# Performance work log

Hardware: AMD Instinct MI355X
Metric: run time of the kernel (lower is better)

Reference implementation:

```python
import jax, jax.numpy as jnp
import numpy as np

B, S, H, T, W = 8, 512, 768, 4, 10
NEG = -1e9

def _u(key, shape, k):
    return jax.random.uniform(key, shape, jnp.float32, -k, k)

def setup_inputs():
    key = jax.random.key(0)
    ks = jax.random.split(key, 20)
    kh = float(1.0 / np.sqrt(H)); kt = float(1.0 / np.sqrt(T))
    return dict(
        embeddings=jax.random.normal(ks[0], (B, S, H), jnp.float32),
        l1f_wih=_u(ks[1], (4 * H, H), kh), l1f_whh=_u(ks[2], (4 * H, H), kh), l1f_b=_u(ks[3], (4 * H,), kh),
        l1r_wih=_u(ks[4], (4 * H, H), kh), l1r_whh=_u(ks[5], (4 * H, H), kh), l1r_b=_u(ks[6], (4 * H,), kh),
        attn_w=_u(ks[7], (3 * H,), kh), attn_b=_u(ks[8], (1,), kh),
        l2f_wih=_u(ks[9], (4 * T, 2 * H), kt), l2f_whh=_u(ks[10], (4 * T, T), kt), l2f_b=_u(ks[11], (4 * T,), kt),
        l2r_wih=_u(ks[12], (4 * T, 2 * H), kt), l2r_whh=_u(ks[13], (4 * T, T), kt), l2r_b=_u(ks[14], (4 * T,), kt),
        crf_start=0.1 * jax.random.normal(ks[15], (T,), jnp.float32),
        crf_end=0.1 * jax.random.normal(ks[16], (T,), jnp.float32),
        crf_trans=0.1 * jax.random.normal(ks[17], (T, T), jnp.float32),
        window_size=W,
    )

def _lstm_dir(x, w_ih, w_hh, b):
    # x: [B,S,D] -> [B,S,Hh]; torch gate order i,f,g,o
    Hh = w_hh.shape[1]
    bs = x.shape[0]
    xs = (jnp.einsum('bsd,gd->bsg', x, w_ih) + b).transpose(1, 0, 2)  # [S,B,4Hh]
    def step(carry, xt):
        h, c = carry
        g = xt + h @ w_hh.T
        i, f, gg, o = jnp.split(g, 4, axis=-1)
        c = jax.nn.sigmoid(f) * c + jax.nn.sigmoid(i) * jnp.tanh(gg)
        h = jax.nn.sigmoid(o) * jnp.tanh(c)
        return (h, c), h
    init = (jnp.zeros((bs, Hh), x.dtype), jnp.zeros((bs, Hh), x.dtype))
    _, hs = jax.lax.scan(step, init, xs)
    return hs.transpose(1, 0, 2)

def _bilstm(x, pf, pr):
    hf = _lstm_dir(x, *pf)
    hr = _lstm_dir(x[:, ::-1], *pr)[:, ::-1]
    return jnp.concatenate([hf, hr], axis=-1)

def _win_attn(h, w, b, win):
    # h: [B,S,D]; similarity(hi,hj) = w1.hi + w2.hj + w3.(hi*hj) + b
    bs, s, d = h.shape
    w1, w2, w3 = w[:d], w[d:2 * d], w[2 * d:]
    offs = jnp.arange(-win, win + 1)                      # [K]
    idx = jnp.arange(s)[:, None] + offs[None, :]          # [S,K]
    valid = (idx >= 0) & (idx < s)
    idxc = jnp.clip(idx, 0, s - 1)
    hw = h[:, idxc]                                       # [B,S,K,D]
    scores = (h @ w1)[:, :, None] \
        + jnp.einsum('bskd,d->bsk', hw, w2) \
        + jnp.einsum('bsd,bskd->bsk', h * w3, hw) + b[0]
    scores = jnp.where(valid[None], scores, NEG)
    aw = jax.nn.softmax(scores, axis=-1)                  # [B,S,K]
    return jnp.einsum('bsk,bskd->bsd', aw, hw)

def _viterbi(em, start, end, trans):
    # em: [B,S,T] -> tags [B,S]
    score0 = start[None] + em[:, 0]
    ems = em.transpose(1, 0, 2)[1:]                       # [S-1,B,T]
    def step(score, e_t):
        nxt = score[:, :, None] + trans[None]             # [B,Tprev,T]
        best = jnp.max(nxt, axis=1) + e_t
        bp = jnp.argmax(nxt, axis=1)
        return best, bp
    final, bps = jax.lax.scan(step, score0, ems)          # bps [S-1,B,T]
    final = final + end[None]
    last = jnp.argmax(final, axis=-1)                     # [B]
    def back(tag, bp):
        prev = jnp.take_along_axis(bp, tag[:, None], axis=1)[:, 0]
        return prev, prev
    _, tags_rev = jax.lax.scan(back, last, bps[::-1])
    return jnp.concatenate([tags_rev[::-1], last[None]], axis=0).transpose(1, 0)

def reference(embeddings, l1f_wih, l1f_whh, l1f_b, l1r_wih, l1r_whh, l1r_b,
              attn_w, attn_b, l2f_wih, l2f_whh, l2f_b, l2r_wih, l2r_whh, l2r_b,
              crf_start, crf_end, crf_trans, window_size):
    h1 = _bilstm(embeddings, (l1f_wih, l1f_whh, l1f_b), (l1r_wih, l1r_whh, l1r_b))
    d = h1.shape[-1] // 2
    hs = h1[..., :d] + h1[..., d:]                        # sum of directions [B,S,H]
    att = _win_attn(hs, attn_w, attn_b, int(window_size))
    x2 = jnp.concatenate([hs, att], axis=-1)              # [B,S,2H]
    h2 = _bilstm(x2, (l2f_wih, l2f_whh, l2f_b), (l2r_wih, l2r_whh, l2r_b))
    d2 = h2.shape[-1] // 2
    em = h2[..., :d2] + h2[..., d2:]                      # CRF emissions [B,S,T]
    tags = _viterbi(em, crf_start, crf_end, crf_trans)
    return tags, em
```

## Files before the change

kernel.cpp:

```cpp
#include <hip/hip_runtime.h>
#include <math.h>

#define SEQ 512
#define BATCH 8
#define HID 768
#define G4 3072
#define CHUNK 128
#define NEGV (-1000000000.0f)

typedef float v4f __attribute__((ext_vector_type(4)));

__device__ __forceinline__ float sigm(float x) { return 1.0f / (1.0f + expf(-x)); }

__device__ __forceinline__ float wred(float x) {
#pragma unroll
  for (int off = 32; off > 0; off >>= 1) x += __shfl_xor(x, off, 64);
  return x;
}

__device__ __forceinline__ void load2_f4_sc(const float* p0, const float* p1,
                                            v4f& a, v4f& b) {
  asm volatile("global_load_dwordx4 %0, %2, off sc0 sc1\n\t"
               "global_load_dwordx4 %1, %3, off sc0 sc1\n\t"
               "s_waitcnt vmcnt(0)"
               : "=&v"(a), "=&v"(b) : "v"(p0), "v"(p1) : "memory");
}
__device__ __forceinline__ int load_i_sc(const int* p) {
  int r;
  asm volatile("global_load_dword %0, %1, off sc0 sc1\n\ts_waitcnt vmcnt(0)"
               : "=v"(r) : "v"(p) : "memory");
  return r;
}
__device__ __forceinline__ void store_f_sc(float* p, float v) {
  asm volatile("global_store_dword %0, %1, off sc0 sc1" :: "v"(p), "v"(v) : "memory");
}
__device__ __forceinline__ void store_i_sc(int* p, int v) {
  asm volatile("global_store_dword %0, %1, off sc0 sc1" :: "v"(p), "v"(v) : "memory");
}

template <int CTRL, int RMASK>
__device__ __forceinline__ float dpp_add(float x) {
  int y = __builtin_amdgcn_update_dpp(0, __float_as_int(x), CTRL, RMASK, 0xF, false);
  return x + __int_as_float(y);
}
__device__ __forceinline__ float reduce32(float x) {
  x = dpp_add<0x121, 0xF>(x);
  x = dpp_add<0x122, 0xF>(x);
  x = dpp_add<0x124, 0xF>(x);
  x = dpp_add<0x128, 0xF>(x);
  x = dpp_add<0x142, 0xA>(x);
  return x;
}

__global__ void k_init(float* __restrict__ hbuf, int* __restrict__ flags) {
  int i = blockIdx.x * blockDim.x + threadIdx.x;
  if (i < 2 * 2 * BATCH * HID) hbuf[i] = 0.0f;
  if (i < 4096) flags[i] = 0;
}

__global__ __launch_bounds__(256) void k_proj1(
    const float* __restrict__ emb,
    const float* __restrict__ w_f, const float* __restrict__ b_f,
    const float* __restrict__ w_r, const float* __restrict__ b_r,
    float* __restrict__ xs_f, float* __restrict__ xs_r, int chunk) {
  __shared__ float As[16][132];
  __shared__ float Bs[16][132];
  const int tid = threadIdx.x;
  const int bn0 = blockIdx.x * 128;
  const int bb  = blockIdx.y;
  const int dir = blockIdx.z;
  const float* W    = dir ? w_r : w_f;
  const float* bias = dir ? b_r : b_f;
  float* xs = dir ? xs_r : xs_f;

  float acc[8][8];
#pragma unroll
  for (int i = 0; i < 8; i++)
#pragma unroll
    for (int j = 0; j < 8; j++) acc[i][j] = 0.0f;

  const int mload = tid & 127;
  const int kq0   = tid >> 7;
  const int tglob = dir ? (SEQ - 1 - (chunk * CHUNK + mload)) : (chunk * CHUNK + mload);
  const float* arow = emb + (size_t)(bb * SEQ + tglob) * HID;
  const float* brow = W + (size_t)(bn0 + mload) * HID;
  const int tm = tid & 15, tn = tid >> 4;

  for (int kt = 0; kt < HID; kt += 16) {
#pragma unroll
    for (int rep = 0; rep < 2; rep++) {
      int kq = kq0 + rep * 2;
      float4 a = *(const float4*)(arow + kt + kq * 4);
      As[kq * 4 + 0][mload] = a.x; As[kq * 4 + 1][mload] = a.y;
      As[kq * 4 + 2][mload] = a.z; As[kq * 4 + 3][mload] = a.w;
      float4 b = *(const float4*)(brow + kt + kq * 4);
      Bs[kq * 4 + 0][mload] = b.x; Bs[kq * 4 + 1][mload] = b.y;
      Bs[kq * 4 + 2][mload] = b.z; Bs[kq * 4 + 3][mload] = b.w;
    }
    __syncthreads();
#pragma unroll
    for (int k = 0; k < 16; k++) {
      float4 a0 = *(const float4*)&As[k][tm * 8];
      float4 a1 = *(const float4*)&As[k][tm * 8 + 4];
      float4 b0 = *(const float4*)&Bs[k][tn * 8];
      float4 b1 = *(const float4*)&Bs[k][tn * 8 + 4];
      float av[8] = {a0.x, a0.y, a0.z, a0.w, a1.x, a1.y, a1.z, a1.w};
      float bv[8] = {b0.x, b0.y, b0.z, b0.w, b1.x, b1.y, b1.z, b1.w};
#pragma unroll
      for (int i = 0; i < 8; i++)
#pragma unroll
        for (int j = 0; j < 8; j++) acc[i][j] += av[i] * bv[j];
    }
    __syncthreads();
  }
#pragma unroll
  for (int i = 0; i < 8; i++) {
    int row = tm * 8 + i;
    size_t base = (size_t)(bb * CHUNK + row) * G4 + bn0 + tn * 8;
#pragma unroll
    for (int j = 0; j < 8; j++) xs[base + j] = acc[i][j] + bias[bn0 + tn * 8 + j];
  }
}

__global__ __launch_bounds__(384, 2) void k_rec1(
    const float* __restrict__ whh_f, const float* __restrict__ whh_r,
    const float* __restrict__ xs_f, const float* __restrict__ xs_r,
    float* __restrict__ hbuf, float* __restrict__ cbuf, int* __restrict__ flags,
    float* __restrict__ hf, float* __restrict__ hr, int t0, int init) {
  __shared__ float hlds[4 * HID];
  const int tid = threadIdx.x;
  const int bid = blockIdx.x;
  const int dir = bid >> 7;
  const int bh  = (bid >> 6) & 1;
  const int jb  = bid & 63;
  const int J0  = jb * 12;
  const int grp = dir * 2 + bh;
  const int g  = tid >> 5;
  const int kq = tid & 31;
  const int j  = J0 + g;

  const float* W  = dir ? whh_r : whh_f;
  const float* xs = dir ? xs_r  : xs_f;
  float* harr = dir ? hr : hf;

  float wreg[4][24];
#pragma unroll
  for (int gate = 0; gate < 4; gate++) {
#pragma unroll
    for (int q = 0; q < 6; q++) {
      *(v4f*)&wreg[gate][q * 4] =
          *(const v4f*)&W[(size_t)(gate * HID + j) * HID + q * 128 + kq * 4];
    }
  }

  float cc[4];
#pragma unroll
  for (int b = 0; b < 4; b++) cc[b] = 0.0f;
  if (!init && kq == 16) {
#pragma unroll
    for (int b = 0; b < 4; b++) cc[b] = cbuf[bid * 48 + g * 4 + b];
  }

  for (int stp = 0; stp < CHUNK; stp++) {
    const int s = t0 + stp;
    const int par = s & 1;

    float xsv[4][4];
    if (kq == 16) {
#pragma unroll
      for (int b = 0; b < 4; b++) {
        const size_t xbase = (size_t)((bh * 4 + b) * CHUNK + stp) * G4 + j;
#pragma unroll
        for (int gate = 0; gate < 4; gate++)
          xsv[b][gate] = xs[xbase + gate * HID];
      }
    }

    if (tid < 64) {
      const int* fp = flags + (grp * 64 + tid) * 16;
      while (load_i_sc(fp) < s) { __builtin_amdgcn_s_sleep(4); }
    }
    __syncthreads();

    {
      const float* src = hbuf + (size_t)((par * 2 + dir) * BATCH + bh * 4) * HID + tid * 8;
      v4f a, b4;
      load2_f4_sc(src, src + 4, a, b4);
      *(v4f*)&hlds[tid * 8]     = a;
      *(v4f*)&hlds[tid * 8 + 4] = b4;
    }
    __syncthreads();

    float acc[4][4];
#pragma unroll
    for (int gate = 0; gate < 4; gate++)
#pragma unroll
      for (int b = 0; b < 4; b++) acc[gate][b] = 0.0f;
#pragma unroll
    for (int b = 0; b < 4; b++) {
      float hk[24];
#pragma unroll
      for (int q = 0; q < 6; q++)
        *(v4f*)&hk[q * 4] = *(const v4f*)&hlds[b * HID + q * 128 + kq * 4];
#pragma unroll
      for (int gate = 0; gate < 4; gate++)
#pragma unroll
        for (int k = 0; k < 24; k++) acc[gate][b] += wreg[gate][k] * hk[k];
    }
#pragma unroll
    for (int gate = 0; gate < 4; gate++)
#pragma unroll
      for (int b = 0; b < 4; b++) acc[gate][b] = reduce32(acc[gate][b]);

    if (kq == 16) {
      const int t = dir ? (SEQ - 1 - s) : s;
#pragma unroll
      for (int b = 0; b < 4; b++) {
        const int bg = bh * 4 + b;
        float iv = acc[0][b] + xsv[b][0];
        float fv = acc[1][b] + xsv[b][1];
        float gv = acc[2][b] + xsv[b][2];
        float ov = acc[3][b] + xsv[b][3];
        cc[b] = sigm(fv) * cc[b] + sigm(iv) * tanhf(gv);
        float h = sigm(ov) * tanhf(cc[b]);
        store_f_sc(hbuf + (size_t)(((par ^ 1) * 2 + dir) * BATCH + bg) * HID + j, h);
        harr[(size_t)(bg * SEQ + t) * HID + j] = h;
      }
    }
    asm volatile("s_waitcnt vmcnt(0)" ::: "memory");
    __syncthreads();
    if (tid == 0) store_i_sc(flags + (grp * 64 + jb) * 16, s + 1);
  }
  if (kq == 16) {
#pragma unroll
    for (int b = 0; b < 4; b++) cbuf[bid * 48 + g * 4 + b] = cc[b];
  }
}

__global__ void k_sum(float* __restrict__ hf, const float* __restrict__ hr) {
  int i = blockIdx.x * 256 + threadIdx.x;
  float4 a = ((const float4*)hf)[i];
  float4 b = ((const float4*)hr)[i];
  a.x += b.x; a.y += b.y; a.z += b.z; a.w += b.w;
  ((float4*)hf)[i] = a;
}

__global__ __launch_bounds__(64) void k_attn(
    const float* __restrict__ hs, const float* __restrict__ attn_w,
    const float* __restrict__ attn_b, float* __restrict__ att) {
  const int l = threadIdx.x;
  const int s = blockIdx.x, b = blockIdx.y;
  const float* hrow = hs + (size_t)(b * SEQ + s) * HID;
  float v[12];
  float u1p = 0.0f;
#pragma unroll
  for (int jj = 0; jj < 12; jj++) {
    int d = l + 64 * jj;
    float x = hrow[d];
    u1p += x * attn_w[d];
    v[jj] = attn_w[HID + d] + x * attn_w[2 * HID + d];
  }
  float u1 = wred(u1p) + attn_b[0];
  float sc[21];
  for (int o = 0; o < 21; o++) {
    int s2 = s + o - 10;
    if (s2 >= 0 && s2 < SEQ) {
      const float* h2 = hs + (size_t)(b * SEQ + s2) * HID;
      float p = 0.0f;
#pragma unroll
      for (int jj = 0; jj < 12; jj++) p += h2[l + 64 * jj] * v[jj];
      sc[o] = wred(p) + u1;
    } else {
      sc[o] = NEGV;
    }
  }
  float m = sc[0];
#pragma unroll
  for (int o = 1; o < 21; o++) m = fmaxf(m, sc[o]);
  float sum = 0.0f;
#pragma unroll
  for (int o = 0; o < 21; o++) { sc[o] = expf(sc[o] - m); sum += sc[o]; }
  float inv = 1.0f / sum;
  float acc[12];
#pragma unroll
  for (int jj = 0; jj < 12; jj++) acc[jj] = 0.0f;
  for (int o = 0; o < 21; o++) {
    int s2 = s + o - 10;
    if (s2 < 0 || s2 >= SEQ) continue;
    float a = sc[o] * inv;
    const float* h2 = hs + (size_t)(b * SEQ + s2) * HID;
#pragma unroll
    for (int jj = 0; jj < 12; jj++) acc[jj] += a * h2[l + 64 * jj];
  }
  float* orow = att + (size_t)(b * SEQ + s) * HID;
#pragma unroll
  for (int jj = 0; jj < 12; jj++) orow[l + 64 * jj] = acc[jj];
}

__global__ __launch_bounds__(256) void k_proj2(
    const float* __restrict__ hs, const float* __restrict__ att,
    const float* __restrict__ w2f, const float* __restrict__ b2f,
    const float* __restrict__ w2r, const float* __restrict__ b2r,
    float* __restrict__ xs2) {
  __shared__ __align__(16) float x2[2 * HID];
  __shared__ float part[32][9];
  const int tid = threadIdx.x;
  const int s = blockIdx.x, b = blockIdx.y;
  size_t base = (size_t)(b * SEQ + s) * HID;
  for (int i = tid; i < 2 * HID; i += 256)
    x2[i] = (i < HID) ? hs[base + i] : att[base + i - HID];
  __syncthreads();
  const int gid = tid & 31, pp = tid >> 5;
  const int d = gid >> 4, g = gid & 15;
  const float4* w4 = (const float4*)((d ? w2r : w2f) + (size_t)g * (2 * HID));
  const float4* x4 = (const float4*)x2;
  float p = 0.0f;
  for (int e = pp * 48; e < pp * 48 + 48; e++) {
    float4 xv = x4[e];
    float4 wv = w4[e];
    p += xv.x * wv.x + xv.y * wv.y + xv.z * wv.z + xv.w * wv.w;
  }
  part[gid][pp] = p;
  __syncthreads();
  if (tid < 32) {
    float sumv = (d ? b2r : b2f)[g];
#pragma unroll
    for (int q = 0; q < 8; q++) sumv += part[gid][q];
    xs2[(size_t)((d * BATCH + b) * SEQ + s) * 16 + g] = sumv;
  }
}

__global__ __launch_bounds__(256) void k_rec2(
    const float* __restrict__ xs2,
    const float* __restrict__ whh_f, const float* __restrict__ whh_r,
    float* __restrict__ h2) {
  __shared__ float hsh[2 * BATCH * 4];
  __shared__ float gsh[2 * BATCH * 16];
  const int tid = threadIdx.x;
  const int d = tid >> 7, b = (tid >> 4) & 7, g = tid & 15;
  const float* whh = (d ? whh_r : whh_f) + g * 4;
  const float w0 = whh[0], w1 = whh[1], w2 = whh[2], w3 = whh[3];
  const int hb = d * BATCH + b;
  if (g < 4) hsh[hb * 4 + g] = 0.0f;
  float c = 0.0f;
  __syncthreads();
  const float* xrow = xs2 + (size_t)hb * SEQ * 16 + g;
  for (int st = 0; st < SEQ; st++) {
    int t = d ? (SEQ - 1 - st) : st;
    float gv = xrow[t * 16] + w0 * hsh[hb * 4 + 0] + w1 * hsh[hb * 4 + 1] +
               w2 * hsh[hb * 4 + 2] + w3 * hsh[hb * 4 + 3];
    gsh[hb * 16 + g] = gv;
    __syncthreads();
    if (g < 4) {
      float iv = gsh[hb * 16 + g];
      float fv = gsh[hb * 16 + 4 + g];
      float gq = gsh[hb * 16 + 8 + g];
      float ov = gsh[hb * 16 + 12 + g];
      c = sigm(fv) * c + sigm(iv) * tanhf(gq);
      float h = sigm(ov) * tanhf(c);
      hsh[hb * 4 + g] = h;
      h2[((size_t)hb * SEQ + t) * 4 + g] = h;
    }
    __syncthreads();
  }
}

__global__ void k_em(const float* __restrict__ h2, float* __restrict__ out) {
  int i = blockIdx.x * 256 + threadIdx.x;
  if (i < BATCH * SEQ * 4) out[BATCH * SEQ + i] = h2[i] + h2[BATCH * SEQ * 4 + i];
}

__global__ __launch_bounds__(32) void k_viterbi(
    float* __restrict__ out, const float* __restrict__ start,
    const float* __restrict__ endw, const float* __restrict__ trans) {
  __shared__ unsigned char bp[SEQ - 1][32];
  const int l = threadIdx.x;
  const int b = l >> 2, j = l & 3;
  const float* em = out + BATCH * SEQ;
  const float tr0 = trans[0 * 4 + j], tr1 = trans[1 * 4 + j];
  const float tr2 = trans[2 * 4 + j], tr3 = trans[3 * 4 + j];
  float score = start[j] + em[((size_t)b * SEQ + 0) * 4 + j];
  for (int t = 1; t < SEQ; t++) {
    float s0 = __shfl(score, b * 4 + 0, 64);
    float s1 = __shfl(score, b * 4 + 1, 64);
    float s2 = __shfl(score, b * 4 + 2, 64);
    float s3 = __shfl(score, b * 4 + 3, 64);
    float v0 = s0 + tr0, v1 = s1 + tr1, v2 = s2 + tr2, v3 = s3 + tr3;
    float best = v0; int arg = 0;
    if (v1 > best) { best = v1; arg = 1; }
    if (v2 > best) { best = v2; arg = 2; }
    if (v3 > best) { best = v3; arg = 3; }
    bp[t - 1][l] = (unsigned char)arg;
    score = best + em[((size_t)b * SEQ + t) * 4 + j];
  }
  score += endw[j];
  float f0 = __shfl(score, b * 4 + 0, 64);
  float f1 = __shfl(score, b * 4 + 1, 64);
  float f2 = __shfl(score, b * 4 + 2, 64);
  float f3 = __shfl(score, b * 4 + 3, 64);
  if (j == 0) {
    float bbv = f0; int last = 0;
    if (f1 > bbv) { bbv = f1; last = 1; }
    if (f2 > bbv) { bbv = f2; last = 2; }
    if (f3 > bbv) { bbv = f3; last = 3; }
    int tag = last;
    out[b * SEQ + (SEQ - 1)] = (float)tag;
    for (int t = SEQ - 2; t >= 0; t--) {
      tag = bp[t][b * 4 + tag];
      out[b * SEQ + t] = (float)tag;
    }
  }
}

extern "C" void kernel_launch(void* const* d_in, const int* in_sizes, int n_in,
                              void* d_out, int out_size, void* d_ws, size_t ws_size,
                              hipStream_t stream) {
  const float* emb      = (const float*)d_in[0];
  const float* l1f_wih  = (const float*)d_in[1];
  const float* l1f_whh  = (const float*)d_in[2];
  const float* l1f_b    = (const float*)d_in[3];
  const float* l1r_wih  = (const float*)d_in[4];
  const float* l1r_whh  = (const float*)d_in[5];
  const float* l1r_b    = (const float*)d_in[6];
  const float* attn_w   = (const float*)d_in[7];
  const float* attn_b   = (const float*)d_in[8];
  const float* l2f_wih  = (const float*)d_in[9];
  const float* l2f_whh  = (const float*)d_in[10];
  const float* l2f_b    = (const float*)d_in[11];
  const float* l2r_wih  = (const float*)d_in[12];
  const float* l2r_whh  = (const float*)d_in[13];
  const float* l2r_b    = (const float*)d_in[14];
  const float* crf_start= (const float*)d_in[15];
  const float* crf_end  = (const float*)d_in[16];
  const float* crf_trans= (const float*)d_in[17];

  float* ws = (float*)d_ws;
  const size_t NCH = (size_t)BATCH * CHUNK * G4;
  float* xs_f = ws;
  float* xs_r = xs_f + NCH;
  float* hf   = xs_r + NCH;
  float* hr   = hf + (size_t)BATCH * SEQ * HID;
  float* hbuf = hr + (size_t)BATCH * SEQ * HID;
  float* cbuf = hbuf + 2 * 2 * BATCH * HID;
  float* h2   = cbuf + 256 * 48;
  int*   flags= (int*)(h2 + 2 * BATCH * SEQ * 4);
  float* xs2  = xs_f;
  float* att  = xs_r;
  float* hs   = hf;

  k_init<<<dim3(96), dim3(256), 0, stream>>>(hbuf, flags);

  for (int c = 0; c < 4; c++) {
    k_proj1<<<dim3(24, 8, 2), dim3(256), 0, stream>>>(
        emb, l1f_wih, l1f_b, l1r_wih, l1r_b, xs_f, xs_r, c);
    k_rec1<<<dim3(256), dim3(384), 0, stream>>>(
        l1f_whh, l1r_whh, xs_f, xs_r, hbuf, cbuf, flags, hf, hr,
        c * CHUNK, c == 0 ? 1 : 0);
  }

  k_sum<<<dim3(3072), dim3(256), 0, stream>>>(hf, hr);
  k_attn<<<dim3(SEQ, BATCH), dim3(64), 0, stream>>>(hs, attn_w, attn_b, att);
  k_proj2<<<dim3(SEQ, BATCH), dim3(256), 0, stream>>>(
      hs, att, l2f_wih, l2f_b, l2r_wih, l2r_b, xs2);
  k_rec2<<<dim3(1), dim3(256), 0, stream>>>(xs2, l2f_whh, l2r_whh, h2);
  k_em<<<dim3(64), dim3(256), 0, stream>>>(h2, (float*)d_out);
  k_viterbi<<<dim3(1), dim3(32), 0, stream>>>((float*)d_out, crf_start, crf_end, crf_trans);
}
```

Baseline: 3.860 ms.

## Fuse next-chunk input projection into recurrent kernel launch with double-buffered gates

Merges the layer-1 input projection for the next chunk into the same launch as the current chunk's recurrence. Extra blocks beyond the 256 recurrent blocks run the GEMM into a second gate buffer, and the two buffers alternate between chunks. This hides the projection time behind the latency-bound recurrence and removes the serial projection launches between chunks. In exchange, the GEMM blocks share CUs and memory bandwidth with the spin-waiting recurrent blocks, which could slow the critical path. The design also relies on the recurrent blocks being co-resident despite the larger grid.

```diff
diff --git a/kernel.cpp b/kernel.cpp
--- a/kernel.cpp
+++ b/kernel.cpp
@@ -122,118 +122,196 @@
   }
 }
 
-__global__ __launch_bounds__(384, 2) void k_rec1(
+__global__ __launch_bounds__(384, 2) void k_fused(
+    const float* __restrict__ emb,
+    const float* __restrict__ w_f, const float* __restrict__ b_f,
+    const float* __restrict__ w_r, const float* __restrict__ b_r,
     const float* __restrict__ whh_f, const float* __restrict__ whh_r,
     const float* __restrict__ xs_f, const float* __restrict__ xs_r,
+    float* __restrict__ xn_f, float* __restrict__ xn_r,
     float* __restrict__ hbuf, float* __restrict__ cbuf, int* __restrict__ flags,
-    float* __restrict__ hf, float* __restrict__ hr, int t0, int init) {
-  __shared__ float hlds[4 * HID];
+    float* __restrict__ hf, float* __restrict__ hr,
+    int t0, int init, int chunk_nxt) {
+  __shared__ __align__(16) float smem[2 * 16 * 132];
   const int tid = threadIdx.x;
-  const int bid = blockIdx.x;
-  const int dir = bid >> 7;
-  const int bh  = (bid >> 6) & 1;
-  const int jb  = bid & 63;
-  const int J0  = jb * 12;
-  const int grp = dir * 2 + bh;
-  const int g  = tid >> 5;
-  const int kq = tid & 31;
-  const int j  = J0 + g;
-
-  const float* W  = dir ? whh_r : whh_f;
-  const float* xs = dir ? xs_r  : xs_f;
-  float* harr = dir ? hr : hf;
-
-  float wreg[4][24];
-#pragma unroll
-  for (int gate = 0; gate < 4; gate++) {
-#pragma unroll
-    for (int q = 0; q < 6; q++) {
-      *(v4f*)&wreg[gate][q * 4] =
-          *(const v4f*)&W[(size_t)(gate * HID + j) * HID + q * 128 + kq * 4];
-    }
-  }
-
-  float cc[4];
-#pragma unroll
-  for (int b = 0; b < 4; b++) cc[b] = 0.0f;
-  if (!init && kq == 16) {
-#pragma unroll
-    for (int b = 0; b < 4; b++) cc[b] = cbuf[bid * 48 + g * 4 + b];
-  }
-
-  for (int stp = 0; stp < CHUNK; stp++) {
-    const int s = t0 + stp;
-    const int par = s & 1;
-
-    float xsv[4][4];
+
+  if (blockIdx.x < 256) {
+    float* hlds = smem;
+    const int bid = blockIdx.x;
+    const int dir = bid >> 7;
+    const int bh  = (bid >> 6) & 1;
+    const int jb  = bid & 63;
+    const int J0  = jb * 12;
+    const int grp = dir * 2 + bh;
+    const int g  = tid >> 5;
+    const int kq = tid & 31;
+    const int j  = J0 + g;
+
+    const float* W  = dir ? whh_r : whh_f;
+    const float* xs = dir ? xs_r  : xs_f;
+    float* harr = dir ? hr : hf;
+
+    float wreg[4][24];
+#pragma unroll
+    for (int gate = 0; gate < 4; gate++) {
+#pragma unroll
+      for (int q = 0; q < 6; q++) {
+        *(v4f*)&wreg[gate][q * 4] =
+            *(const v4f*)&W[(size_t)(gate * HID + j) * HID + q * 128 + kq * 4];
+      }
+    }
+
+    float cc[4];
+#pragma unroll
+    for (int b = 0; b < 4; b++) cc[b] = 0.0f;
+    if (!init && kq == 16) {
+#pragma unroll
+      for (int b = 0; b < 4; b++) cc[b] = cbuf[bid * 48 + g * 4 + b];
+    }
+
+    for (int stp = 0; stp < CHUNK; stp++) {
+      const int s = t0 + stp;
+      const int par = s & 1;
+
+      float xsv[4][4];
+      if (kq == 16) {
+#pragma unroll
+        for (int b = 0; b < 4; b++) {
+          const size_t xbase = (size_t)((bh * 4 + b) * CHUNK + stp) * G4 + j;
+#pragma unroll
+          for (int gate = 0; gate < 4; gate++)
+            xsv[b][gate] = xs[xbase + gate * HID];
+        }
+      }
+
+      if (tid < 64) {
+        const int* fp = flags + (grp * 64 + tid) * 16;
+        while (load_i_sc(fp) < s) { __builtin_amdgcn_s_sleep(4); }
+      }
+      __syncthreads();
+
+      {
+        const float* src = hbuf + (size_t)((par * 2 + dir) * BATCH + bh * 4) * HID + tid * 8;
+        v4f a, b4;
+        load2_f4_sc(src, src + 4, a, b4);
+        *(v4f*)&hlds[tid * 8]     = a;
+        *(v4f*)&hlds[tid * 8 + 4] = b4;
+      }
+      __syncthreads();
+
+      float acc[4][4];
+#pragma unroll
+      for (int gate = 0; gate < 4; gate++)
+#pragma unroll
+        for (int b = 0; b < 4; b++) acc[gate][b] = 0.0f;
+#pragma unroll
+      for (int b = 0; b < 4; b++) {
+        float hk[24];
+#pragma unroll
+        for (int q = 0; q < 6; q++)
+          *(v4f*)&hk[q * 4] = *(const v4f*)&hlds[b * HID + q * 128 + kq * 4];
+#pragma unroll
+        for (int gate = 0; gate < 4; gate++)
+#pragma unroll
+          for (int k = 0; k < 24; k++) acc[gate][b] += wreg[gate][k] * hk[k];
+      }
+#pragma unroll
+      for (int gate = 0; gate < 4; gate++)
+#pragma unroll
+        for (int b = 0; b < 4; b++) acc[gate][b] = reduce32(acc[gate][b]);
+
+      if (kq == 16) {
+        const int t = dir ? (SEQ - 1 - s) : s;
+#pragma unroll
+        for (int b = 0; b < 4; b++) {
+          const int bg = bh * 4 + b;
+          float iv = acc[0][b] + xsv[b][0];
+          float fv = acc[1][b] + xsv[b][1];
+          float gv = acc[2][b] + xsv[b][2];
+          float ov = acc[3][b] + xsv[b][3];
+          cc[b] = sigm(fv) * cc[b] + sigm(iv) * tanhf(gv);
+          float h = sigm(ov) * tanhf(cc[b]);
+          store_f_sc(hbuf + (size_t)(((par ^ 1) * 2 + dir) * BATCH + bg) * HID + j, h);
+          harr[(size_t)(bg * SEQ + t) * HID + j] = h;
+        }
+      }
+      asm volatile("s_waitcnt vmcnt(0)" ::: "memory");
+      __syncthreads();
+      if (tid == 0) store_i_sc(flags + (grp * 64 + jb) * 16, s + 1);
+    }
     if (kq == 16) {
 #pragma unroll
-      for (int b = 0; b < 4; b++) {
-        const size_t xbase = (size_t)((bh * 4 + b) * CHUNK + stp) * G4 + j;
-#pragma unroll
-        for (int gate = 0; gate < 4; gate++)
-          xsv[b][gate] = xs[xbase + gate * HID];
-      }
-    }
-
-    if (tid < 64) {
-      const int* fp = flags + (grp * 64 + tid) * 16;
-      while (load_i_sc(fp) < s) { __builtin_amdgcn_s_sleep(4); }
-    }
-    __syncthreads();
-
-    {
-      const float* src = hbuf + (size_t)((par * 2 + dir) * BATCH + bh * 4) * HID + tid * 8;
-      v4f a, b4;
-      load2_f4_sc(src, src + 4, a, b4);
-      *(v4f*)&hlds[tid * 8]     = a;
-      *(v4f*)&hlds[tid * 8 + 4] = b4;
-    }
-    __syncthreads();
-
-    float acc[4][4];
-#pragma unroll
-    for (int gate = 0; gate < 4; gate++)
-#pragma unroll
-      for (int b = 0; b < 4; b++) acc[gate][b] = 0.0f;
-#pragma unroll
-    for (int b = 0; b < 4; b++) {
-      float hk[24];
-#pragma unroll
-      for (int q = 0; q < 6; q++)
-        *(v4f*)&hk[q * 4] = *(const v4f*)&hlds[b * HID + q * 128 + kq * 4];
-#pragma unroll
-      for (int gate = 0; gate < 4; gate++)
-#pragma unroll
-        for (int k = 0; k < 24; k++) acc[gate][b] += wreg[gate][k] * hk[k];
-    }
-#pragma unroll
-    for (int gate = 0; gate < 4; gate++)
-#pragma unroll
-      for (int b = 0; b < 4; b++) acc[gate][b] = reduce32(acc[gate][b]);
-
-    if (kq == 16) {
-      const int t = dir ? (SEQ - 1 - s) : s;
-#pragma unroll
-      for (int b = 0; b < 4; b++) {
-        const int bg = bh * 4 + b;
-        float iv = acc[0][b] + xsv[b][0];
-        float fv = acc[1][b] + xsv[b][1];
-        float gv = acc[2][b] + xsv[b][2];
-        float ov = acc[3][b] + xsv[b][3];
-        cc[b] = sigm(fv) * cc[b] + sigm(iv) * tanhf(gv);
-        float h = sigm(ov) * tanhf(cc[b]);
-        store_f_sc(hbuf + (size_t)(((par ^ 1) * 2 + dir) * BATCH + bg) * HID + j, h);
-        harr[(size_t)(bg * SEQ + t) * HID + j] = h;
-      }
-    }
-    asm volatile("s_waitcnt vmcnt(0)" ::: "memory");
-    __syncthreads();
-    if (tid == 0) store_i_sc(flags + (grp * 64 + jb) * 16, s + 1);
-  }
-  if (kq == 16) {
-#pragma unroll
-    for (int b = 0; b < 4; b++) cbuf[bid * 48 + g * 4 + b] = cc[b];
+      for (int b = 0; b < 4; b++) cbuf[bid * 48 + g * 4 + b] = cc[b];
+    }
+  } else {
+    if (chunk_nxt < 0) return;
+    float (*As)[132] = (float(*)[132])smem;
+    float (*Bs)[132] = (float(*)[132])&smem[16 * 132];
+
+    int p = blockIdx.x - 256;
+    const int dirz = p / 192; p -= dirz * 192;
+    const int bb = p / 24;
+    const int bx = p - bb * 24;
+    const int bn0 = bx * 128;
+
+    const float* W    = dirz ? w_r : w_f;
+    const float* bias = dirz ? b_r : b_f;
+    float* xs = dirz ? xn_r : xn_f;
+
+    float acc[8][8];
+#pragma unroll
+    for (int i = 0; i < 8; i++)
+#pragma unroll
+      for (int j = 0; j < 8; j++) acc[i][j] = 0.0f;
+
+    const int mload = tid & 127;
+    const int kq0   = tid >> 7;
+    const int tglob = dirz ? (SEQ - 1 - (chunk_nxt * CHUNK + mload))
+                           : (chunk_nxt * CHUNK + mload);
+    const float* arow = emb + (size_t)(bb * SEQ + tglob) * HID;
+    const float* brow = W + (size_t)(bn0 + mload) * HID;
+    const int tm = tid & 15, tn = tid >> 4;
+
+    for (int kt = 0; kt < HID; kt += 16) {
+      if (tid < 256) {
+#pragma unroll
+        for (int rep = 0; rep < 2; rep++) {
+          int kq = kq0 + rep * 2;
+          float4 a = *(const float4*)(arow + kt + kq * 4);
+          As[kq * 4 + 0][mload] = a.x; As[kq * 4 + 1][mload] = a.y;
+          As[kq * 4 + 2][mload] = a.z; As[kq * 4 + 3][mload] = a.w;
+          float4 b = *(const float4*)(brow + kt + kq * 4);
+          Bs[kq * 4 + 0][mload] = b.x; Bs[kq * 4 + 1][mload] = b.y;
+          Bs[kq * 4 + 2][mload] = b.z; Bs[kq * 4 + 3][mload] = b.w;
+        }
+      }
+      __syncthreads();
+      if (tid < 256) {
+#pragma unroll
+        for (int k = 0; k < 16; k++) {
+          float4 a0 = *(const float4*)&As[k][tm * 8];
+          float4 a1 = *(const float4*)&As[k][tm * 8 + 4];
+          float4 b0 = *(const float4*)&Bs[k][tn * 8];
+          float4 b1 = *(const float4*)&Bs[k][tn * 8 + 4];
+          float av[8] = {a0.x, a0.y, a0.z, a0.w, a1.x, a1.y, a1.z, a1.w};
+          float bv[8] = {b0.x, b0.y, b0.z, b0.w, b1.x, b1.y, b1.z, b1.w};
+#pragma unroll
+          for (int i = 0; i < 8; i++)
+#pragma unroll
+            for (int j = 0; j < 8; j++) acc[i][j] += av[i] * bv[j];
+        }
+      }
+      __syncthreads();
+    }
+    if (tid < 256) {
+#pragma unroll
+      for (int i = 0; i < 8; i++) {
+        int row = tm * 8 + i;
+        size_t base = (size_t)(bb * CHUNK + row) * G4 + bn0 + tn * 8;
+#pragma unroll
+        for (int j = 0; j < 8; j++) xs[base + j] = acc[i][j] + bias[bn0 + tn * 8 + j];
+      }
+    }
   }
 }
 
@@ -436,26 +514,35 @@
 
   float* ws = (float*)d_ws;
   const size_t NCH = (size_t)BATCH * CHUNK * G4;
-  float* xs_f = ws;
-  float* xs_r = xs_f + NCH;
-  float* hf   = xs_r + NCH;
+  float* xs_f0 = ws;
+  float* xs_r0 = xs_f0 + NCH;
+  float* xs_f1 = xs_r0 + NCH;
+  float* xs_r1 = xs_f1 + NCH;
+  float* hf   = xs_r1 + NCH;
   float* hr   = hf + (size_t)BATCH * SEQ * HID;
   float* hbuf = hr + (size_t)BATCH * SEQ * HID;
   float* cbuf = hbuf + 2 * 2 * BATCH * HID;
   float* h2   = cbuf + 256 * 48;
   int*   flags= (int*)(h2 + 2 * BATCH * SEQ * 4);
-  float* xs2  = xs_f;
-  float* att  = xs_r;
+  float* xs2  = xs_f0;
+  float* att  = xs_r0;
   float* hs   = hf;
 
   k_init<<<dim3(96), dim3(256), 0, stream>>>(hbuf, flags);
 
+  k_proj1<<<dim3(24, 8, 2), dim3(256), 0, stream>>>(
+      emb, l1f_wih, l1f_b, l1r_wih, l1r_b, xs_f0, xs_r0, 0);
+
   for (int c = 0; c < 4; c++) {
-    k_proj1<<<dim3(24, 8, 2), dim3(256), 0, stream>>>(
-        emb, l1f_wih, l1f_b, l1r_wih, l1r_b, xs_f, xs_r, c);
-    k_rec1<<<dim3(256), dim3(384), 0, stream>>>(
-        l1f_whh, l1r_whh, xs_f, xs_r, hbuf, cbuf, flags, hf, hr,
-        c * CHUNK, c == 0 ? 1 : 0);
+    const float* xcf = (c & 1) ? xs_f1 : xs_f0;
+    const float* xcr = (c & 1) ? xs_r1 : xs_r0;
+    float* xnf = (c & 1) ? xs_f0 : xs_f1;
+    float* xnr = (c & 1) ? xs_r0 : xs_r1;
+    const int nblk = (c < 3) ? (256 + 384) : 256;
+    k_fused<<<dim3(nblk), dim3(384), 0, stream>>>(
+        emb, l1f_wih, l1f_b, l1r_wih, l1r_b, l1f_whh, l1r_whh,
+        xcf, xcr, xnf, xnr, hbuf, cbuf, flags, hf, hr,
+        c * CHUNK, c == 0 ? 1 : 0, (c < 3) ? c + 1 : -1);
   }
 
   k_sum<<<dim3(3072), dim3(256), 0, stream>>>(hf, hr);
```

Measured after the change: 4.123 ms. +6.8%, slower.
